# Performance work log

Measured on AMD Instinct MI355X. Metric: run time of the kernel, lower is better.

## Reference

```python
import jax, jax.numpy as jnp
import numpy as np

L, D, F, V = 24, 1024, 4096, 50277  # n_layer, n_embd, ffn hidden (4*D), vocab
RESCALE = 6


def _ln(x, w, b, eps=1e-5):
    m = jnp.mean(x, axis=-1, keepdims=True)
    v = jnp.mean(jnp.square(x - m), axis=-1, keepdims=True)
    return (x - m) * jax.lax.rsqrt(v + eps) * w + b


def setup_inputs() -> dict:
    key = jax.random.key(0)
    ks = iter(jax.random.split(key, 64))

    def nrm(shape, s=0.02):
        return jax.random.normal(next(ks), shape, jnp.float32) * s

    def uni(shape):
        return jax.random.uniform(next(ks), shape, jnp.float32)

    state = jnp.zeros((L, 5, D), jnp.float32).at[:, 4, :].set(-1e30)  # pp init
    return {
        "token_embd": jax.random.normal(next(ks), (D,), jnp.float32),
        "state": state,
        "emb_ln_w": jnp.ones((D,), jnp.float32),
        "emb_ln_b": jnp.zeros((D,), jnp.float32),
        "ln1_w": jnp.ones((L, D), jnp.float32),
        "ln1_b": jnp.zeros((L, D), jnp.float32),
        "ln2_w": jnp.ones((L, D), jnp.float32),
        "ln2_b": jnp.zeros((L, D), jnp.float32),
        "att_tmk": uni((L, D)),
        "att_tmv": uni((L, D)),
        "att_tmr": uni((L, D)),
        "att_tf": nrm((L, D), 0.5),
        "att_td": -jnp.exp(nrm((L, D), 0.5)),  # time_decay = -exp(w) at load
        "att_kw": nrm((L, D, D)),
        "att_vw": nrm((L, D, D)),
        "att_rw": nrm((L, D, D)),
        "att_ow": nrm((L, D, D)),
        "ffn_tmk": uni((L, D)),
        "ffn_tmr": uni((L, D)),
        "ffn_kw": nrm((L, F, D)),
        "ffn_vw": nrm((L, D, F)),
        "ffn_rw": nrm((L, D, D)),
        "out_ln_w": jnp.ones((D,), jnp.float32),
        "out_ln_b": jnp.zeros((D,), jnp.float32),
        "head_w": nrm((V, D)),
    }


def reference(token_embd, state, emb_ln_w, emb_ln_b, ln1_w, ln1_b, ln2_w, ln2_b,
              att_tmk, att_tmv, att_tmr, att_tf, att_td, att_kw, att_vw, att_rw,
              att_ow, ffn_tmk, ffn_tmr, ffn_kw, ffn_vw, ffn_rw,
              out_ln_w, out_ln_b, head_w):
    x0 = _ln(token_embd, emb_ln_w, emb_ln_b)  # encoder

    def layer(x, inputs):
        (i, st, l1w, l1b, l2w, l2b, tmk, tmv, tmr, tf, td,
         kw, vw, rw, ow, ftmk, ftmr, fkw, fvw, frw) = inputs
        # ---- time mixing ----
        xn = _ln(x, l1w, l1b)
        s_att, aa, bb, pp = st[1], st[2], st[3], st[4]
        xk = xn * tmk + s_att * (1 - tmk)
        xv = xn * tmv + s_att * (1 - tmv)
        xr = xn * tmr + s_att * (1 - tmr)
        r = jax.nn.sigmoid(rw @ xr)
        kk = kw @ xk
        vv = vw @ xv
        ww = tf + kk
        p = jnp.maximum(pp, ww)
        e1 = jnp.exp(pp - p)
        e2 = jnp.exp(ww - p)
        a = e1 * aa + e2 * vv
        b = e1 * bb + e2
        ww2 = pp + td
        p2 = jnp.maximum(ww2, kk)
        f1 = jnp.exp(ww2 - p2)
        f2 = jnp.exp(kk - p2)
        new_aa = f1 * aa + f2 * vv
        new_bb = f1 * bb + f2
        x = x + ow @ (r * (a / b))
        # ---- channel mixing ----
        xn2 = _ln(x, l2w, l2b)
        s_ffn = st[0]
        xk2 = xn2 * ftmk + s_ffn * (1 - ftmk)
        xr2 = xn2 * ftmr + s_ffn * (1 - ftmr)
        r2 = jax.nn.sigmoid(frw @ xr2)
        k2 = jnp.square(jax.nn.relu(fkw @ xk2))
        x = x + r2 * (fvw @ k2)
        # rescale every RESCALE layers
        x = jnp.where((i + 1) % RESCALE == 0, x * 0.5, x)
        new_st = jnp.stack([xn2, xn, new_aa, new_bb, p2])
        return x, new_st

    idx = jnp.arange(L)
    x, new_state = jax.lax.scan(
        layer, x0,
        (idx, state, ln1_w, ln1_b, ln2_w, ln2_b, att_tmk, att_tmv, att_tmr,
         att_tf, att_td, att_kw, att_vw, att_rw, att_ow, ffn_tmk, ffn_tmr,
         ffn_kw, ffn_vw, ffn_rw))
    logits = head_w @ _ln(x, out_ln_w, out_ln_b)  # decoder
    return logits, new_state
```

## Files before the change

kernel.cpp:

```cpp
#include <hip/hip_runtime.h>

#define DD 1024
#define FF 4096
#define LL 24
#define VV 50277
#define NB 1024
#define AG __HIP_MEMORY_SCOPE_AGENT

typedef unsigned u32;
typedef float v4f __attribute__((ext_vector_type(4)));


__device__ __forceinline__ float wave_sum(float v) {
#pragma unroll
    for (int o = 32; o > 0; o >>= 1) v += __shfl_xor(v, o, 64);
    return v;
}

__device__ __forceinline__ v4f ln_fast(v4f x, const float* __restrict__ w,
                                       const float* __restrict__ b,
                                       float* scr, int t) {
    float s1 = x[0] + x[1] + x[2] + x[3];
    float s2 = x[0]*x[0] + x[1]*x[1] + x[2]*x[2] + x[3]*x[3];
    s1 = wave_sum(s1); s2 = wave_sum(s2);
    int wv = t >> 6;
    __syncthreads();
    if ((t & 63) == 0) { scr[wv] = s1; scr[4 + wv] = s2; }
    __syncthreads();
    float S1 = scr[0] + scr[1] + scr[2] + scr[3];
    float S2 = scr[4] + scr[5] + scr[6] + scr[7];
    float m = S1 * (1.0f / 1024.0f);
    float var = S2 * (1.0f / 1024.0f) - m * m;
    float rs = rsqrtf(var + 1e-5f);
    v4f w4 = ((const v4f*)w)[t], b4 = ((const v4f*)b)[t];
    return (x - m) * rs * w4 + b4;
}

__device__ __forceinline__ v4f mixv(v4f n, v4f s, v4f m) { return n * m + s * (1.0f - m); }

__device__ __forceinline__ float dotv(v4f a, v4f x) {
    return fmaf(a[0], x[0], fmaf(a[1], x[1], fmaf(a[2], x[2], a[3] * x[3])));
}

struct Row { v4f a, b, c, d; };

__device__ __forceinline__ void row_load(Row& r, const float* p, int lane) {
    const v4f* q = (const v4f*)p;
    r.a = q[lane]; r.b = q[lane + 64]; r.c = q[lane + 128]; r.d = q[lane + 192];
}
__device__ __forceinline__ void row_pin(Row& r) {
    asm volatile("" : "+v"(r.a), "+v"(r.b), "+v"(r.c), "+v"(r.d));
}
__device__ __forceinline__ float row_dot(const Row& r, const v4f* v, int lane) {
    return dotv(r.a, v[lane]) + dotv(r.b, v[lane + 64]) +
           dotv(r.c, v[lane + 128]) + dotv(r.d, v[lane + 192]);
}


__device__ __forceinline__ void astore_f(float* p, float v) {
    __hip_atomic_store(p, v, __ATOMIC_RELAXED, AG);
}
__device__ __forceinline__ void cload(v4f& d, const float* p) {
    asm volatile("global_load_dwordx4 %0, %1, off sc0 sc1" : "=v"(d) : "v"(p));
}
__device__ __forceinline__ void cwait1(v4f& a) {
    asm volatile("s_waitcnt vmcnt(0)" : "+v"(a));
}
__device__ __forceinline__ void cwait4(v4f& a, v4f& b, v4f& c, v4f& d) {
    asm volatile("s_waitcnt vmcnt(0)" : "+v"(a), "+v"(b), "+v"(c), "+v"(d));
}


__device__ __forceinline__ void gbar(u32* sync, u32 ev, int b, int t) {
    __syncthreads();
    if (t == 0) {
        u32* shard = sync + (b & 7) * 32;
        u32* l2c   = sync + 8 * 32;
        u32* rel0  = sync + 9 * 32;
        u32 old = __hip_atomic_fetch_add(shard, 1u, __ATOMIC_RELAXED, AG);
        if (old == 128u * ev - 1u) {
            u32 o2 = __hip_atomic_fetch_add(l2c, 1u, __ATOMIC_RELAXED, AG);
            if (o2 == 8u * ev - 1u) {
#pragma unroll
                for (int i = 0; i < 8; ++i)
                    __hip_atomic_store(rel0 + i * 32, ev, __ATOMIC_RELAXED, AG);
            }
        }
        u32* myrel = rel0 + (b & 7) * 32;
        while (__hip_atomic_load(myrel, __ATOMIC_RELAXED, AG) < ev)
            __builtin_amdgcn_s_sleep(2);
    }
    __syncthreads();
}


__global__ __launch_bounds__(256, 4) void rwkv_all(
    const float* __restrict__ token_embd, const float* __restrict__ state,
    const float* __restrict__ emb_ln_w, const float* __restrict__ emb_ln_b,
    const float* __restrict__ ln1_w, const float* __restrict__ ln1_b,
    const float* __restrict__ ln2_w, const float* __restrict__ ln2_b,
    const float* __restrict__ att_tmk, const float* __restrict__ att_tmv,
    const float* __restrict__ att_tmr, const float* __restrict__ att_tf,
    const float* __restrict__ att_td,
    const float* __restrict__ att_kw, const float* __restrict__ att_vw,
    const float* __restrict__ att_rw, const float* __restrict__ att_ow,
    const float* __restrict__ ffn_tmk, const float* __restrict__ ffn_tmr,
    const float* __restrict__ ffn_kw, const float* __restrict__ ffn_vw,
    const float* __restrict__ ffn_rw,
    const float* __restrict__ out_ln_w, const float* __restrict__ out_ln_b,
    const float* __restrict__ head_w,
    float* __restrict__ logits, float* __restrict__ st_out_base,
    float* __restrict__ ws, u32* __restrict__ sync) {

    __shared__ __align__(16) v4f s_buf[1024];
    __shared__ __align__(16) v4f s_vec[256];
    __shared__ float scr[8];
    __shared__ float s_kvr[3];
    __shared__ float s_part[8];
    __shared__ float s_xsave;

    const int t = threadIdx.x, lane = t & 63, w = t >> 6, b = blockIdx.x;

    float* rab = ws;
    float* xB  = ws + 1024;
    float* k2  = ws + 2048;
    float* xD  = ws + 6144;

    Row rA;
    row_load(rA, (w == 0 ? att_kw : w == 1 ? att_vw : w == 2 ? att_rw : att_ow)
                 + (size_t)b * DD, lane);
    row_pin(rA);

    v4f xv = ((const v4f*)token_embd)[t];
    xv = ln_fast(xv, emb_ln_w, emb_ln_b, scr, t);

    u32 ev = 0;
#pragma unroll 1
    for (int i = 0; i < LL; ++i) {
        const size_t oD = (size_t)i * DD;
        const float* st = state + (size_t)i * 5 * DD;
        float* sto = st_out_base + (size_t)i * 5 * DD;
        const float scale = ((i + 1) % 6 == 0) ? 0.5f : 1.0f;

        if (i > 0) { cload(xv, xD + 4 * t); cwait1(xv); }
        if (t == (b >> 2)) s_xsave = xv[b & 3];
        v4f n = ln_fast(xv, ln1_w + oD, ln1_b + oD, scr, t);
        if (b == 0) ((v4f*)(sto + DD))[t] = n;
        {
            v4f sa = ((const v4f*)(st + DD))[t];
            s_buf[t]       = mixv(n, sa, ((const v4f*)(att_tmk + oD))[t]);
            s_buf[256 + t] = mixv(n, sa, ((const v4f*)(att_tmv + oD))[t]);
            s_buf[512 + t] = mixv(n, sa, ((const v4f*)(att_tmr + oD))[t]);
        }
        __syncthreads();
        if (w < 3) {
            float acc = wave_sum(row_dot(rA, &s_buf[w * 256], lane));
            if (lane == 0) s_kvr[w] = acc;
        }
        __syncthreads();
        if (t == 0) {
            float kk = s_kvr[0], vv = s_kvr[1];
            float rr = 1.0f / (1.0f + expf(-s_kvr[2]));
            float aa = st[2 * DD + b], bb = st[3 * DD + b], pp = st[4 * DD + b];
            float ww = att_tf[oD + b] + kk;
            float p = fmaxf(pp, ww);
            float e1 = expf(pp - p), e2 = expf(ww - p);
            astore_f(rab + b, rr * ((e1 * aa + e2 * vv) / (e1 * bb + e2)));
            float ww2 = pp + att_td[oD + b];
            float p2 = fmaxf(ww2, kk);
            float f1 = expf(ww2 - p2), f2 = expf(kk - p2);
            sto[2 * DD + b] = f1 * aa + f2 * vv;
            sto[3 * DD + b] = f1 * bb + f2;
            sto[4 * DD + b] = p2;
        }
        Row rFK;
        row_load(rFK, ffn_kw + (size_t)i * FF * DD + (size_t)(4 * b + w) * DD, lane);
        row_pin(rFK);
        gbar(sync, ++ev, b, t);

        { v4f rv; cload(rv, rab + 4 * t); cwait1(rv); s_vec[t] = rv; }
        __syncthreads();
        if (w == 3) {
            float acc = wave_sum(row_dot(rA, &s_vec[0], lane));
            if (lane == 0) astore_f(xB + b, s_xsave + acc);
        }
        v4f frq = ((const v4f*)(ffn_rw + (size_t)i * DD * DD + (size_t)b * DD))[w * 64 + lane];
        asm volatile("" : "+v"(frq));
        gbar(sync, ++ev, b, t);

        cload(xv, xB + 4 * t); cwait1(xv);
        if (t == (b >> 2)) s_xsave = xv[b & 3];
        n = ln_fast(xv, ln2_w + oD, ln2_b + oD, scr, t);
        if (b == 0) ((v4f*)sto)[t] = n;
        {
            v4f sf = ((const v4f*)st)[t];
            s_buf[t]       = mixv(n, sf, ((const v4f*)(ffn_tmk + oD))[t]);
            s_buf[256 + t] = mixv(n, sf, ((const v4f*)(ffn_tmr + oD))[t]);
        }
        __syncthreads();
        {
            float acc = wave_sum(row_dot(rFK, &s_buf[0], lane));
            if (lane == 0) { float rl = fmaxf(acc, 0.f); astore_f(k2 + 4 * b + w, rl * rl); }
            float pr = wave_sum(dotv(frq, s_buf[256 + w * 64 + lane]));
            if (lane == 0) s_part[w] = pr;
        }
        Row rFV;
        row_load(rFV, ffn_vw + (size_t)i * DD * FF + (size_t)b * FF + (size_t)w * 1024, lane);
        row_pin(rFV);
        gbar(sync, ++ev, b, t);

        {
            v4f q0, q1, q2, q3;
            cload(q0, k2 + 4 * t);        cload(q1, k2 + 4 * t + 1024);
            cload(q2, k2 + 4 * t + 2048); cload(q3, k2 + 4 * t + 3072);
            cwait4(q0, q1, q2, q3);
            s_buf[t] = q0; s_buf[256 + t] = q1; s_buf[512 + t] = q2; s_buf[768 + t] = q3;
        }
        __syncthreads();
        {
            float acc = 0.f;
            acc += dotv(rFV.a, s_buf[w * 256 + lane]);
            acc += dotv(rFV.b, s_buf[w * 256 + lane + 64]);
            acc += dotv(rFV.c, s_buf[w * 256 + lane + 128]);
            acc += dotv(rFV.d, s_buf[w * 256 + lane + 192]);
            acc = wave_sum(acc);
            if (lane == 0) s_part[4 + w] = acc;
        }
        __syncthreads();
        if (t == 0) {
            float r2v = 1.0f / (1.0f + expf(-(s_part[0] + s_part[1] + s_part[2] + s_part[3])));
            float dsum = s_part[4] + s_part[5] + s_part[6] + s_part[7];
            astore_f(xD + b, (s_xsave + r2v * dsum) * scale);
        }
        if (i + 1 < LL) {
            row_load(rA, (w == 0 ? att_kw : w == 1 ? att_vw : w == 2 ? att_rw : att_ow)
                         + (size_t)(i + 1) * DD * DD + (size_t)b * DD, lane);
            row_pin(rA);
        }
        gbar(sync, ++ev, b, t);
    }

    cload(xv, xD + 4 * t); cwait1(xv);
    v4f nh = ln_fast(xv, out_ln_w, out_ln_b, scr, t);
    s_vec[t] = nh;
    __syncthreads();
#pragma unroll 1
    for (int j = 0; j < 13; ++j) {
        int row = j * 4096 + 4 * b + w;
        if (row < VV) {
            Row rh;
            row_load(rh, head_w + (size_t)row * DD, lane);
            float acc = wave_sum(row_dot(rh, &s_vec[0], lane));
            if (lane == 0) logits[row] = acc;
        }
    }
}


extern "C" void kernel_launch(void* const* d_in, const int* in_sizes, int n_in,
                              void* d_out, int out_size, void* d_ws, size_t ws_size,
                              hipStream_t stream) {
    const float* token_embd = (const float*)d_in[0];
    const float* state      = (const float*)d_in[1];
    const float* emb_ln_w   = (const float*)d_in[2];
    const float* emb_ln_b   = (const float*)d_in[3];
    const float* ln1_w      = (const float*)d_in[4];
    const float* ln1_b      = (const float*)d_in[5];
    const float* ln2_w      = (const float*)d_in[6];
    const float* ln2_b      = (const float*)d_in[7];
    const float* att_tmk    = (const float*)d_in[8];
    const float* att_tmv    = (const float*)d_in[9];
    const float* att_tmr    = (const float*)d_in[10];
    const float* att_tf     = (const float*)d_in[11];
    const float* att_td     = (const float*)d_in[12];
    const float* att_kw     = (const float*)d_in[13];
    const float* att_vw     = (const float*)d_in[14];
    const float* att_rw     = (const float*)d_in[15];
    const float* att_ow     = (const float*)d_in[16];
    const float* ffn_tmk    = (const float*)d_in[17];
    const float* ffn_tmr    = (const float*)d_in[18];
    const float* ffn_kw     = (const float*)d_in[19];
    const float* ffn_vw     = (const float*)d_in[20];
    const float* ffn_rw     = (const float*)d_in[21];
    const float* out_ln_w   = (const float*)d_in[22];
    const float* out_ln_b   = (const float*)d_in[23];
    const float* head_w     = (const float*)d_in[24];

    float* logits = (float*)d_out;
    float* st_out_base = (float*)d_out + VV;

    float* ws = (float*)d_ws;
    u32* sync = (u32*)(ws + 8192);

    hipMemsetAsync(sync, 0, 4096, stream);

    rwkv_all<<<NB, 256, 0, stream>>>(
        token_embd, state, emb_ln_w, emb_ln_b, ln1_w, ln1_b, ln2_w, ln2_b,
        att_tmk, att_tmv, att_tmr, att_tf, att_td,
        att_kw, att_vw, att_rw, att_ow,
        ffn_tmk, ffn_tmr, ffn_kw, ffn_vw, ffn_rw,
        out_ln_w, out_ln_b, head_w,
        logits, st_out_base, ws, sync);
}
```

Before: 695.4 us.

## Split grid barrier into arrive/wait and prefetch weights between phases

Splits the grid barrier into separate arrive and wait halves so the next phase's weight-row loads are issued while blocks wait for the barrier release. Work is redistributed across waves: wave 0 stays idle, and waves 1-3 each hold up to two pinned rows for the k/v/r, ffn-key, ffn-receptance and ffn-value matvecs. The head projection is software-pipelined by loading the next row before computing the current one. The cost is that fewer waves do the dot products and each active wave needs more registers.

```diff
diff --git a/kernel.cpp b/kernel.cpp
--- a/kernel.cpp
+++ b/kernel.cpp
@@ -71,7 +71,7 @@
 }
 
 
-__device__ __forceinline__ void gbar(u32* sync, u32 ev, int b, int t) {
+__device__ __forceinline__ void bar_arrive(u32* sync, u32 ev, int b, int t) {
     __syncthreads();
     if (t == 0) {
         u32* shard = sync + (b & 7) * 32;
@@ -86,7 +86,14 @@
                     __hip_atomic_store(rel0 + i * 32, ev, __ATOMIC_RELAXED, AG);
             }
         }
-        u32* myrel = rel0 + (b & 7) * 32;
+    }
+    __builtin_amdgcn_sched_barrier(0);
+}
+
+__device__ __forceinline__ void bar_wait(u32* sync, u32 ev, int b, int t) {
+    __builtin_amdgcn_sched_barrier(0);
+    if (t == 0) {
+        u32* myrel = sync + 9 * 32 + (b & 7) * 32;
         while (__hip_atomic_load(myrel, __ATOMIC_RELAXED, AG) < ev)
             __builtin_amdgcn_s_sleep(2);
     }
@@ -126,10 +133,12 @@
     float* k2  = ws + 2048;
     float* xD  = ws + 6144;
 
-    Row rA;
-    row_load(rA, (w == 0 ? att_kw : w == 1 ? att_vw : w == 2 ? att_rw : att_ow)
-                 + (size_t)b * DD, lane);
-    row_pin(rA);
+    Row rA, rB;
+    if (w == 2)      { row_load(rA, att_kw + (size_t)b * DD, lane);
+                       row_load(rB, att_vw + (size_t)b * DD, lane); }
+    else if (w == 1)   row_load(rA, att_rw + (size_t)b * DD, lane);
+    else if (w == 3)   row_load(rA, att_ow + (size_t)b * DD, lane);
+    if (w) { row_pin(rA); }
 
     v4f xv = ((const v4f*)token_embd)[t];
     xv = ln_fast(xv, emb_ln_w, emb_ln_b, scr, t);
@@ -153,9 +162,13 @@
             s_buf[512 + t] = mixv(n, sa, ((const v4f*)(att_tmr + oD))[t]);
         }
         __syncthreads();
-        if (w < 3) {
-            float acc = wave_sum(row_dot(rA, &s_buf[w * 256], lane));
-            if (lane == 0) s_kvr[w] = acc;
+        if (w == 2) {
+            float a0 = wave_sum(row_dot(rA, &s_buf[0], lane));
+            float a1 = wave_sum(row_dot(rB, &s_buf[256], lane));
+            if (lane == 0) { s_kvr[0] = a0; s_kvr[1] = a1; }
+        } else if (w == 1) {
+            float a2 = wave_sum(row_dot(rA, &s_buf[512], lane));
+            if (lane == 0) s_kvr[2] = a2;
         }
         __syncthreads();
         if (t == 0) {
@@ -173,10 +186,13 @@
             sto[3 * DD + b] = f1 * bb + f2;
             sto[4 * DD + b] = p2;
         }
-        Row rFK;
-        row_load(rFK, ffn_kw + (size_t)i * FF * DD + (size_t)(4 * b + w) * DD, lane);
-        row_pin(rFK);
-        gbar(sync, ++ev, b, t);
+        bar_arrive(sync, ++ev, b, t);
+        if (w == 1) {
+            const float* fk = ffn_kw + (size_t)i * FF * DD + (size_t)(4 * b) * DD;
+            row_load(rA, fk, lane); row_load(rB, fk + DD, lane);
+            row_pin(rA); row_pin(rB);
+        }
+        bar_wait(sync, ev, b, t);
 
         { v4f rv; cload(rv, rab + 4 * t); cwait1(rv); s_vec[t] = rv; }
         __syncthreads();
@@ -184,9 +200,16 @@
             float acc = wave_sum(row_dot(rA, &s_vec[0], lane));
             if (lane == 0) astore_f(xB + b, s_xsave + acc);
         }
-        v4f frq = ((const v4f*)(ffn_rw + (size_t)i * DD * DD + (size_t)b * DD))[w * 64 + lane];
-        asm volatile("" : "+v"(frq));
-        gbar(sync, ++ev, b, t);
+        bar_arrive(sync, ++ev, b, t);
+        if (w == 3) {
+            const float* fk = ffn_kw + (size_t)i * FF * DD + (size_t)(4 * b + 2) * DD;
+            row_load(rA, fk, lane); row_load(rB, fk + DD, lane);
+            row_pin(rA); row_pin(rB);
+        } else if (w == 2) {
+            row_load(rA, ffn_rw + (size_t)i * DD * DD + (size_t)b * DD, lane);
+            row_pin(rA);
+        }
+        bar_wait(sync, ev, b, t);
 
         cload(xv, xB + 4 * t); cwait1(xv);
         if (t == (b >> 2)) s_xsave = xv[b & 3];
@@ -198,16 +221,35 @@
             s_buf[256 + t] = mixv(n, sf, ((const v4f*)(ffn_tmr + oD))[t]);
         }
         __syncthreads();
+        if (w == 1) {
+            float a0 = wave_sum(row_dot(rA, &s_buf[0], lane));
+            float a1 = wave_sum(row_dot(rB, &s_buf[0], lane));
+            if (lane == 0) {
+                float r0 = fmaxf(a0, 0.f), r1 = fmaxf(a1, 0.f);
+                astore_f(k2 + 4 * b + 0, r0 * r0);
+                astore_f(k2 + 4 * b + 1, r1 * r1);
+            }
+        } else if (w == 3) {
+            float a2 = wave_sum(row_dot(rA, &s_buf[0], lane));
+            float a3 = wave_sum(row_dot(rB, &s_buf[0], lane));
+            if (lane == 0) {
+                float r2_ = fmaxf(a2, 0.f), r3 = fmaxf(a3, 0.f);
+                astore_f(k2 + 4 * b + 2, r2_ * r2_);
+                astore_f(k2 + 4 * b + 3, r3 * r3);
+            }
+        } else if (w == 2) {
+            float ar = wave_sum(row_dot(rA, &s_buf[256], lane));
+            if (lane == 0) s_part[5] = 1.0f / (1.0f + expf(-ar));
+        }
+        bar_arrive(sync, ++ev, b, t);
         {
-            float acc = wave_sum(row_dot(rFK, &s_buf[0], lane));
-            if (lane == 0) { float rl = fmaxf(acc, 0.f); astore_f(k2 + 4 * b + w, rl * rl); }
-            float pr = wave_sum(dotv(frq, s_buf[256 + w * 64 + lane]));
-            if (lane == 0) s_part[w] = pr;
-        }
-        Row rFV;
-        row_load(rFV, ffn_vw + (size_t)i * DD * FF + (size_t)b * FF + (size_t)w * 1024, lane);
-        row_pin(rFV);
-        gbar(sync, ++ev, b, t);
+            const float* fv = ffn_vw + (size_t)i * DD * FF + (size_t)b * FF;
+            if (w == 1) { row_load(rA, fv, lane); row_load(rB, fv + 1024, lane);
+                          row_pin(rA); row_pin(rB); }
+            else if (w == 3) { row_load(rA, fv + 2048, lane); row_load(rB, fv + 3072, lane);
+                               row_pin(rA); row_pin(rB); }
+        }
+        bar_wait(sync, ev, b, t);
 
         {
             v4f q0, q1, q2, q3;
@@ -217,41 +259,51 @@
             s_buf[t] = q0; s_buf[256 + t] = q1; s_buf[512 + t] = q2; s_buf[768 + t] = q3;
         }
         __syncthreads();
-        {
-            float acc = 0.f;
-            acc += dotv(rFV.a, s_buf[w * 256 + lane]);
-            acc += dotv(rFV.b, s_buf[w * 256 + lane + 64]);
-            acc += dotv(rFV.c, s_buf[w * 256 + lane + 128]);
-            acc += dotv(rFV.d, s_buf[w * 256 + lane + 192]);
-            acc = wave_sum(acc);
-            if (lane == 0) s_part[4 + w] = acc;
+        if (w == 1) {
+            float p0 = wave_sum(row_dot(rA, &s_buf[0], lane));
+            float p1 = wave_sum(row_dot(rB, &s_buf[256], lane));
+            if (lane == 0) { s_part[0] = p0; s_part[1] = p1; }
+        } else if (w == 3) {
+            float p2 = wave_sum(row_dot(rA, &s_buf[512], lane));
+            float p3 = wave_sum(row_dot(rB, &s_buf[768], lane));
+            if (lane == 0) { s_part[2] = p2; s_part[3] = p3; }
         }
         __syncthreads();
         if (t == 0) {
-            float r2v = 1.0f / (1.0f + expf(-(s_part[0] + s_part[1] + s_part[2] + s_part[3])));
-            float dsum = s_part[4] + s_part[5] + s_part[6] + s_part[7];
-            astore_f(xD + b, (s_xsave + r2v * dsum) * scale);
-        }
+            float dsum = s_part[0] + s_part[1] + s_part[2] + s_part[3];
+            astore_f(xD + b, (s_xsave + s_part[5] * dsum) * scale);
+        }
+        bar_arrive(sync, ++ev, b, t);
         if (i + 1 < LL) {
-            row_load(rA, (w == 0 ? att_kw : w == 1 ? att_vw : w == 2 ? att_rw : att_ow)
-                         + (size_t)(i + 1) * DD * DD + (size_t)b * DD, lane);
-            row_pin(rA);
-        }
-        gbar(sync, ++ev, b, t);
+            const size_t nxt = (size_t)(i + 1) * DD * DD + (size_t)b * DD;
+            if (w == 2)      { row_load(rA, att_kw + nxt, lane);
+                               row_load(rB, att_vw + nxt, lane);
+                               row_pin(rA); row_pin(rB); }
+            else if (w == 1) { row_load(rA, att_rw + nxt, lane); row_pin(rA); }
+            else if (w == 3) { row_load(rA, att_ow + nxt, lane); row_pin(rA); }
+        }
+        bar_wait(sync, ev, b, t);
     }
 
     cload(xv, xD + 4 * t); cwait1(xv);
     v4f nh = ln_fast(xv, out_ln_w, out_ln_b, scr, t);
     s_vec[t] = nh;
     __syncthreads();
+    {
+        Row rh;
+        int row = 4 * b + w;
+        row_load(rh, head_w + (size_t)row * DD, lane);
 #pragma unroll 1
-    for (int j = 0; j < 13; ++j) {
-        int row = j * 4096 + 4 * b + w;
-        if (row < VV) {
-            Row rh;
-            row_load(rh, head_w + (size_t)row * DD, lane);
-            float acc = wave_sum(row_dot(rh, &s_vec[0], lane));
-            if (lane == 0) logits[row] = acc;
+        for (int j = 0; j < 13; ++j) {
+            Row rn;
+            int nrow = row + 4096;
+            if (j + 1 < 13 && nrow < VV)
+                row_load(rn, head_w + (size_t)nrow * DD, lane);
+            if (row < VV) {
+                float acc = wave_sum(row_dot(rh, &s_vec[0], lane));
+                if (lane == 0) logits[row] = acc;
+            }
+            rh = rn; row = nrow;
         }
     }
 }
```

Measured after the change: 643.5 us. 7.5% less time.
